# Kernel optimization log

Hardware: AMD Instinct MI355X
Metric: run time of the kernel (lower is better)

The kernel has to match this reference:

```python
import jax, jax.numpy as jnp
import numpy as np

# ---- static config (matches init_kwargs) ----
L, MM = 4, 2                     # lmax, mmax
C = 128                          # sphere_channels
H = 64                           # hidden_channels
OUTC = 128                       # output_channels
NH, AC = 8, 64                   # num_heads, attn_alpha_channels
MAXZ = 90
N_NODES, N_EDGES = 1000, 10000
EDGE_CH = 128
X_EDGE = EDGE_CH + 2 * EDGE_CH   # 384 (dist basis + src/tgt atom embeddings)
C3 = 3 * C                       # 384 channels of the concatenated message
EXTRA = NH * AC + L * H          # 768 extra m0 channels (alpha + gates)
M0_OUT = EXTRA + H * (L + 1)     # 1088
NC_FULL = (L + 1) ** 2           # 25

# ---- coefficient bookkeeping (CoefficientMappingModule) ----
_full = [(l, m) for l in range(L + 1) for m in range(-l, l + 1)]
_red = [(l, m) for l in range(L + 1) for m in range(-min(l, MM), min(l, MM) + 1)]
MASK = np.array([_full.index(p) for p in _red])  # rows of wigner with |m|<=mmax
_perm = [i for i, (l, m) in enumerate(_red) if m == 0]
for _mm in range(1, MM + 1):
    _perm += [i for i, (l, m) in enumerate(_red) if m == _mm]
    _perm += [i for i, (l, m) in enumerate(_red) if m == -_mm]
PERM_M = np.array(_perm)                 # l-primary -> m-primary
INV_PERM = np.argsort(PERM_M)            # m-primary -> l-primary
EXPAND_FULL = np.array([l for l, m in _full])       # l of each full coeff
GATE_EXPAND = np.array([l - 1 for l, m in _red if l > 0])


def _ln(h, g, b):
    mu = jnp.mean(h, -1, keepdims=True)
    var = jnp.var(h, -1, keepdims=True)
    return (h - mu) / jnp.sqrt(var + 1e-5) * g + b


def _forward(x, edge_fea, edge_distance, wigner, src_emb, tgt_emb,
             rad_w1, rad_b1, rad_g1, rad_bb1, rad_w2, rad_b2, rad_g2, rad_bb2,
             rad_w3, rad_b3, w_m0, b_m0, w_m1, w_m2, proj_w, proj_b,
             atomic_numbers, edge_index):
    E = edge_index.shape[1]
    src, tgt = edge_index[0], edge_index[1]
    # atom-edge embedding concat
    x_edge = jnp.concatenate([edge_distance,
                              src_emb[atomic_numbers[src]],
                              tgt_emb[atomic_numbers[tgt]]], axis=1)     # [E, 384]
    # edge-wise gather + concat -> message [E, 25, 3C]
    msg = jnp.concatenate([x[src], x[tgt], edge_fea], axis=2)
    # radial MLP (Linear + LayerNorm + SiLU, final Linear)
    h = jax.nn.silu(_ln(x_edge @ rad_w1.T + rad_b1, rad_g1, rad_bb1))
    h = jax.nn.silu(_ln(h @ rad_w2.T + rad_b2, rad_g2, rad_bb2))
    w_rad = (h @ rad_w3.T + rad_b3).reshape(E, L + 1, C3)                # [E, 5, 3C]
    msg = msg * w_rad[:, EXPAND_FULL, :]                                 # shared per-l radial weight
    # Wigner rotation restricted to |m| <= mmax: [E, 19, 3C]
    msg = jnp.einsum('emn,enc->emc', wigner[:, MASK, :], msg)
    # SO2 convolution (m-primary layout)
    mp = msg[:, PERM_M, :]
    x0 = mp[:, :L + 1, :].reshape(E, -1) @ w_m0.T + b_m0                 # [E, 1088]
    x0_extra = x0[:, :EXTRA]
    outs = [x0[:, EXTRA:].reshape(E, L + 1, H)]
    off = L + 1
    for m, w in ((1, w_m1), (2, w_m2)):
        nl = L - m + 1
        xm = mp[:, off:off + 2 * nl, :].reshape(E, 2, nl * C3)           # rows: +m, -m
        ym = xm @ w.T                                                    # [E, 2, 2*H*nl]
        half = ym.shape[-1] // 2
        yr, yi = ym[..., :half], ym[..., half:]
        outs.append(jnp.stack([yr[:, 0] - yi[:, 1], yr[:, 1] + yi[:, 0]],
                              axis=1).reshape(E, 2 * nl, H))
        off += 2 * nl
    hl = jnp.concatenate(outs, axis=1)[:, INV_PERM, :]                   # l-primary [E, 19, H]
    # gate activation: sigmoid gates for l>=1, SiLU on scalars
    gating = jax.nn.sigmoid(x0_extra[:, NH * AC:]).reshape(E, L, H)[:, GATE_EXPAND, :]
    hl = jnp.concatenate([jax.nn.silu(hl[:, :1, :]), hl[:, 1:, :] * gating], axis=1)
    # inverse rotation back to full (lmax+1)^2 coefficients: [E, 25, H]
    full = jnp.einsum('emn,emc->enc', wigner[:, MASK, :], hl)
    # SO3_LinearV2: per-l linear, bias only on l=0
    out = jnp.einsum('emi,moi->emo', full, proj_w[EXPAND_FULL])
    out = out.at[:, 0, :].add(proj_b)
    return out


def setup_inputs() -> dict:
    ks = jax.random.split(jax.random.key(0), 16)
    f32 = jnp.float32
    def nrm(k, shape, fan_in):
        return jax.random.normal(k, shape, dtype=f32) * (fan_in ** -0.5)
    return {
        'x': jax.random.normal(ks[0], (N_NODES, NC_FULL, C), dtype=f32),
        'edge_fea': jax.random.normal(ks[1], (N_EDGES, NC_FULL, C), dtype=f32),
        'edge_distance': jax.random.normal(ks[2], (N_EDGES, EDGE_CH), dtype=f32),
        'wigner': nrm(ks[3], (N_EDGES, NC_FULL, NC_FULL), NC_FULL),
        'src_emb': jax.random.uniform(ks[4], (MAXZ, EDGE_CH), f32, -0.001, 0.001),
        'tgt_emb': jax.random.uniform(ks[5], (MAXZ, EDGE_CH), f32, -0.001, 0.001),
        'rad_w1': nrm(ks[6], (EDGE_CH, X_EDGE), X_EDGE),
        'rad_b1': jnp.zeros((EDGE_CH,), f32),
        'rad_g1': jnp.ones((EDGE_CH,), f32),
        'rad_bb1': jnp.zeros((EDGE_CH,), f32),
        'rad_w2': nrm(ks[7], (EDGE_CH, EDGE_CH), EDGE_CH),
        'rad_b2': jnp.zeros((EDGE_CH,), f32),
        'rad_g2': jnp.ones((EDGE_CH,), f32),
        'rad_bb2': jnp.zeros((EDGE_CH,), f32),
        'rad_w3': nrm(ks[8], ((L + 1) * C3, EDGE_CH), EDGE_CH),
        'rad_b3': jnp.zeros(((L + 1) * C3,), f32),
        'w_m0': nrm(ks[9], (M0_OUT, (L + 1) * C3), (L + 1) * C3),
        'b_m0': jnp.zeros((M0_OUT,), f32),
        'w_m1': nrm(ks[10], (2 * H * L, L * C3), L * C3),
        'w_m2': nrm(ks[11], (2 * H * (L - 1), (L - 1) * C3), (L - 1) * C3),
        'proj_w': nrm(ks[12], (L + 1, OUTC, H), H),
        'proj_b': jnp.zeros((OUTC,), f32),
        'atomic_numbers': jax.random.randint(ks[13], (N_NODES,), 0, MAXZ, dtype=jnp.int32),
        'edge_index': jax.random.randint(ks[14], (2, N_EDGES), 0, N_NODES, dtype=jnp.int32),
    }


def reference(x, edge_fea, edge_distance, wigner, src_emb, tgt_emb,
              rad_w1, rad_b1, rad_g1, rad_bb1, rad_w2, rad_b2, rad_g2, rad_bb2,
              rad_w3, rad_b3, w_m0, b_m0, w_m1, w_m2, proj_w, proj_b,
              atomic_numbers, edge_index):
    return _forward(x, edge_fea, edge_distance, wigner, src_emb, tgt_emb,
                    rad_w1, rad_b1, rad_g1, rad_bb1, rad_w2, rad_b2, rad_g2, rad_bb2,
                    rad_w3, rad_b3, w_m0, b_m0, w_m1, w_m2, proj_w, proj_b,
                    atomic_numbers, edge_index)
```

## Files before the change

kernel.cpp:

```cpp
#include <hip/hip_runtime.h>
#include <hip/hip_bf16.h>
#include <stdint.h>


__constant__ int c_MASKP[19] = {0,2,6,12,20, 3,7,13,21, 1,5,11,19, 8,14,22, 4,10,18};
__constant__ int c_GATEP[19] = {-1,0,1,2,3, 0,1,2,3, 0,1,2,3, 1,2,3, 1,2,3};
__constant__ int c_LFULL[25] = {0,1,1,1,2,2,2,2,2,3,3,3,3,3,3,3,4,4,4,4,4,4,4,4,4};

__device__ __forceinline__ float sigm_(float x) { return 1.f / (1.f + __expf(-x)); }

typedef __attribute__((ext_vector_type(8))) __bf16 bf16x8;
typedef __attribute__((ext_vector_type(4))) float floatx4;

__device__ __forceinline__ void async16(const void* g, void* l) {
    __builtin_amdgcn_global_load_lds(
        (__attribute__((address_space(1))) void*)(g),
        (__attribute__((address_space(3))) void*)(l), 16, 0, 0);
}

__global__ void k_split_pw(const float* __restrict__ pw, __hip_bfloat16* __restrict__ pwb) {
    int d = blockIdx.x * 256 + threadIdx.x;
    if (d >= 40960) return;
    int ll = d >> 13, rem = d & 8191;
    int o = rem >> 6, i = rem & 63;
    float v = pw[d];
    __hip_bfloat16 hi = __float2bfloat16(v);
    __hip_bfloat16 lo = __float2bfloat16(v - __bfloat162float(hi));
    long ob = (long)(ll * 128 + o) * 192;
    pwb[ob + i]       = hi;
    pwb[ob + 64 + i]  = lo;
    pwb[ob + 128 + i] = hi;
}

__global__ void k_cvt_w(const float* __restrict__ W, __hip_bfloat16* __restrict__ out,
                        int rows, int rowsPad, int K) {
    long i = (long)blockIdx.x * 256 + threadIdx.x;
    if (i >= (long)rowsPad * K) return;
    int r = (int)(i / K);
    out[i] = __float2bfloat16(r < rows ? W[i] : 0.f);
}

__global__ void k_cvt_w_split(const float* __restrict__ W, __hip_bfloat16* __restrict__ out,
                              int rows, int K) {
    long i = (long)blockIdx.x * 256 + threadIdx.x;
    if (i >= (long)rows * K) return;
    int r = (int)(i / K), k = (int)(i - (long)r * K);
    float v = W[i];
    __hip_bfloat16 hi = __float2bfloat16(v);
    __hip_bfloat16 lo = __float2bfloat16(v - __bfloat162float(hi));
    long ob = (long)r * 3 * K;
    out[ob + k]         = hi;
    out[ob + K + k]     = lo;
    out[ob + 2 * K + k] = hi;
}

__global__ __launch_bounds__(256) void k_build_xedge(
    const float* __restrict__ ed, const float* __restrict__ se, const float* __restrict__ te,
    const int* __restrict__ an, const int* __restrict__ eidx,
    __hip_bfloat16* __restrict__ xeb, int e0, int ec, int E)
{
    long i = (long)blockIdx.x * 256 + threadIdx.x;
    if (i >= (long)ec * 384) return;
    int le = (int)(i / 384), c = (int)(i - (long)le * 384);
    int e = e0 + le;
    float v;
    if (c < 128)       v = ed[(long)e * 128 + c];
    else if (c < 256)  { int s = eidx[e];     v = se[an[s] * 128 + (c - 128)]; }
    else               { int t = eidx[E + e]; v = te[an[t] * 128 + (c - 256)]; }
    __hip_bfloat16 hi = __float2bfloat16(v);
    __hip_bfloat16 lo = __float2bfloat16(v - __bfloat162float(hi));
    long ob = (long)le * 1152;
    xeb[ob + c]       = hi;
    xeb[ob + 384 + c] = hi;
    xeb[ob + 768 + c] = lo;
}

__global__ __launch_bounds__(256) void k_ln_silu(
    const float* __restrict__ H, const float* __restrict__ g, const float* __restrict__ bb,
    __hip_bfloat16* __restrict__ out, int ec, int split)
{
    int row = blockIdx.x * 4 + (threadIdx.x >> 6);
    if (row >= ec) return;
    int lane = threadIdx.x & 63;
    const float* hr = H + (long)row * 128;
    float v0 = hr[lane], v1 = hr[lane + 64];
    float s = v0 + v1, s2 = v0 * v0 + v1 * v1;
    #pragma unroll
    for (int o = 32; o >= 1; o >>= 1) {
        s  += __shfl_xor(s, o, 64);
        s2 += __shfl_xor(s2, o, 64);
    }
    float mu = s * (1.f / 128.f);
    float rs = rsqrtf(s2 * (1.f / 128.f) - mu * mu + 1e-5f);
    float a0 = (v0 - mu) * rs * g[lane]      + bb[lane];
    float a1 = (v1 - mu) * rs * g[lane + 64] + bb[lane + 64];
    a0 = a0 * sigm_(a0);
    a1 = a1 * sigm_(a1);
    if (split) {
        long ob = (long)row * 384;
        __hip_bfloat16 h0 = __float2bfloat16(a0);
        __hip_bfloat16 l0 = __float2bfloat16(a0 - __bfloat162float(h0));
        __hip_bfloat16 h1 = __float2bfloat16(a1);
        __hip_bfloat16 l1 = __float2bfloat16(a1 - __bfloat162float(h1));
        out[ob + lane]            = h0;
        out[ob + 128 + lane]      = h0;
        out[ob + 256 + lane]      = l0;
        out[ob + lane + 64]       = h1;
        out[ob + 128 + lane + 64] = h1;
        out[ob + 256 + lane + 64] = l1;
    } else {
        long ob = (long)row * 128;
        out[ob + lane]      = __float2bfloat16(a0);
        out[ob + lane + 64] = __float2bfloat16(a1);
    }
}

__global__ __launch_bounds__(256) void k_mfma_gemm(
    const __hip_bfloat16* __restrict__ A,
    const __hip_bfloat16* __restrict__ B,
    const float* __restrict__ bias,
    float* __restrict__ Out, int ldo,
    int realM, int realN, int K)
{
    __shared__ __align__(16) __hip_bfloat16 As[128 * 32];
    __shared__ __align__(16) __hip_bfloat16 Bs[128 * 32];
    int tid = threadIdx.x;
    int l = tid & 63, w = tid >> 6;
    int r0 = blockIdx.x * 128, n0 = blockIdx.y * 128;
    int wm = w & 1, wn = w >> 1;

    floatx4 acc[4][4] = {};

    int srow = w * 16 + (l >> 2);
    int scol = (l & 3) * 8;
    const __hip_bfloat16* Ag = A + (long)(r0 + srow) * K + scol;
    const __hip_bfloat16* Bg = B + (long)(n0 + srow) * K + scol;
    __hip_bfloat16* AsW = As + (w * 16) * 32;
    __hip_bfloat16* BsW = Bs + (w * 16) * 32;

    int lrow = l & 15, lk = (l >> 4) * 8;

    for (int kk = 0; kk < K; kk += 32) {
        async16(Ag + kk, AsW);
        async16(Ag + (long)64 * K + kk, AsW + 64 * 32);
        async16(Bg + kk, BsW);
        async16(Bg + (long)64 * K + kk, BsW + 64 * 32);
        __syncthreads();
        bf16x8 af[4], bf[4];
        #pragma unroll
        for (int mi = 0; mi < 4; ++mi)
            af[mi] = *(const bf16x8*)&As[(wm * 64 + mi * 16 + lrow) * 32 + lk];
        #pragma unroll
        for (int ni = 0; ni < 4; ++ni)
            bf[ni] = *(const bf16x8*)&Bs[(wn * 64 + ni * 16 + lrow) * 32 + lk];
        #pragma unroll
        for (int mi = 0; mi < 4; ++mi)
            #pragma unroll
            for (int ni = 0; ni < 4; ++ni)
                acc[mi][ni] = __builtin_amdgcn_mfma_f32_16x16x32_bf16(
                    af[mi], bf[ni], acc[mi][ni], 0, 0, 0);
        __syncthreads();
    }

    int lq = l >> 4;
    #pragma unroll
    for (int ni = 0; ni < 4; ++ni) {
        int col = n0 + wn * 64 + ni * 16 + lrow;
        if (col >= realN) continue;
        float bv = bias ? bias[col] : 0.f;
        #pragma unroll
        for (int mi = 0; mi < 4; ++mi) {
            int rbase = r0 + wm * 64 + mi * 16 + lq * 4;
            floatx4 v = acc[mi][ni];
            #pragma unroll
            for (int r = 0; r < 4; ++r) {
                int row = rbase + r;
                if (row < realM) Out[(long)row * ldo + col] = v[r] + bv;
            }
        }
    }
}

__global__ __launch_bounds__(384) void k_build_mp(
    const float* __restrict__ x, const float* __restrict__ ef, const float* __restrict__ wgn,
    const float* __restrict__ wrad, const int* __restrict__ eidx,
    __hip_bfloat16* __restrict__ A0, __hip_bfloat16* __restrict__ A1,
    __hip_bfloat16* __restrict__ A2, int e0, int E)
{
    __shared__ __align__(16) float swig[512];
    int tid = threadIdx.x;
    int le = blockIdx.x;
    long e = e0 + le;
    int src = eidx[e], tgt = eidx[E + e];

    for (int i = tid; i < 500; i += 384) {
        int n = i / 20, j = i - n * 20;
        swig[i] = (j < 19) ? wgn[e * 625 + c_MASKP[j] * 25 + n] : 0.f;
    }

    int c = tid;
    const float* base;
    if (c < 128)      base = x  + (long)src * 3200 + c;
    else if (c < 256) base = x  + (long)tgt * 3200 + (c - 128);
    else              base = ef + e * 3200 + (c - 256);

    float vals[25];
    #pragma unroll
    for (int n = 0; n < 25; ++n) vals[n] = base[n * 128];
    float rad[5];
    #pragma unroll
    for (int l = 0; l < 5; ++l) rad[l] = wrad[(long)le * 1920 + l * 384 + c];
    #pragma unroll
    for (int n = 0; n < 25; ++n) vals[n] *= rad[c_LFULL[n]];

    __syncthreads();
    const float4* sw = (const float4*)swig;

    float acc[20] = {};
    #pragma unroll
    for (int n = 0; n < 25; ++n) {
        float v = vals[n];
        #pragma unroll
        for (int q = 0; q < 5; ++q) {
            float4 wv = sw[n * 5 + q];
            acc[q * 4 + 0] += wv.x * v;
            acc[q * 4 + 1] += wv.y * v;
            acc[q * 4 + 2] += wv.z * v;
            acc[q * 4 + 3] += wv.w * v;
        }
    }

    #pragma unroll
    for (int j = 0; j < 19; ++j) {
        __hip_bfloat16 hv = __float2bfloat16(acc[j]);
        if (j < 5)       A0[(long)le * 1920 + j * 384 + c] = hv;
        else if (j < 9)  A1[(long)(2 * le)     * 1536 + (j - 5)  * 384 + c] = hv;
        else if (j < 13) A1[(long)(2 * le + 1) * 1536 + (j - 9)  * 384 + c] = hv;
        else if (j < 16) A2[(long)(2 * le)     * 1152 + (j - 13) * 384 + c] = hv;
        else             A2[(long)(2 * le + 1) * 1152 + (j - 16) * 384 + c] = hv;
    }
}

__global__ __launch_bounds__(256) void k_combine_a(
    const float* __restrict__ wgn, const float* __restrict__ ym0,
    const float* __restrict__ ym1, const float* __restrict__ ym2,
    __hip_bfloat16* __restrict__ sfl, int e0, int CE)
{
    __shared__ __align__(16) float swig[512];
    __shared__ float shl[1216];
    int tid = threadIdx.x;
    int le = blockIdx.x;
    long e = e0 + le;

    for (int i = tid; i < 500; i += 256) {
        int n = i / 20, j = i - n * 20;
        swig[i] = (j < 19) ? wgn[e * 625 + c_MASKP[j] * 25 + n] : 0.f;
    }

    const float* y0  = ym0 + (long)le * 576;
    const float* y1a = ym1 + (long)(2 * le) * 512;
    const float* y1b = ym1 + (long)(2 * le + 1) * 512;
    const float* y2a = ym2 + (long)(2 * le) * 384;
    const float* y2b = ym2 + (long)(2 * le + 1) * 384;

    for (int i = tid; i < 1216; i += 256) {
        int j = i >> 6, c = i & 63;
        float raw;
        if (j < 5)        raw = y0[256 + j * 64 + c];
        else if (j < 9)   { int k = (j - 5) * 64 + c;  raw = y1a[k] - y1b[256 + k]; }
        else if (j < 13)  { int k = (j - 9) * 64 + c;  raw = y1b[k] + y1a[256 + k]; }
        else if (j < 16)  { int k = (j - 13) * 64 + c; raw = y2a[k] - y2b[192 + k]; }
        else              { int k = (j - 16) * 64 + c; raw = y2b[k] + y2a[192 + k]; }
        float v;
        if (j == 0) v = raw * sigm_(raw);
        else        v = raw * sigm_(y0[c_GATEP[j] * 64 + c]);
        shl[i] = v;
    }
    __syncthreads();

    for (int i = tid; i < 1600; i += 256) {
        int n = i >> 6, c = i & 63;
        const float4* sw = (const float4*)swig + n * 5;
        float acc = 0.f;
        float4 w0 = sw[0], w1 = sw[1], w2 = sw[2], w3 = sw[3], w4 = sw[4];
        acc += w0.x * shl[ 0 * 64 + c];
        acc += w0.y * shl[ 1 * 64 + c];
        acc += w0.z * shl[ 2 * 64 + c];
        acc += w0.w * shl[ 3 * 64 + c];
        acc += w1.x * shl[ 4 * 64 + c];
        acc += w1.y * shl[ 5 * 64 + c];
        acc += w1.z * shl[ 6 * 64 + c];
        acc += w1.w * shl[ 7 * 64 + c];
        acc += w2.x * shl[ 8 * 64 + c];
        acc += w2.y * shl[ 9 * 64 + c];
        acc += w2.z * shl[10 * 64 + c];
        acc += w2.w * shl[11 * 64 + c];
        acc += w3.x * shl[12 * 64 + c];
        acc += w3.y * shl[13 * 64 + c];
        acc += w3.z * shl[14 * 64 + c];
        acc += w3.w * shl[15 * 64 + c];
        acc += w4.x * shl[16 * 64 + c];
        acc += w4.y * shl[17 * 64 + c];
        acc += w4.z * shl[18 * 64 + c];
        __hip_bfloat16 hi = __float2bfloat16(acc);
        __hip_bfloat16 lo = __float2bfloat16(acc - __bfloat162float(hi));
        int l = c_LFULL[n];
        int nb = l * l, cnt = 2 * l + 1, ni = n - nb;
        long row = (long)CE * nb + (long)le * cnt + ni;
        sfl[row * 192 + c]       = hi;
        sfl[row * 192 + 64 + c]  = hi;
        sfl[row * 192 + 128 + c] = lo;
    }
}

__global__ __launch_bounds__(256) void k_proj_gemm(
    const __hip_bfloat16* __restrict__ sfl,
    const __hip_bfloat16* __restrict__ pwb,
    const float* __restrict__ pb,
    float* __restrict__ out, int ec, int CE)
{
    __shared__ __align__(16) __hip_bfloat16 As[128 * 32];
    __shared__ __align__(16) __hip_bfloat16 Bs[128 * 32];
    int tid = threadIdx.x;
    int ln = tid & 63, w = tid >> 6;
    int wm = w & 1, wn = w >> 1;

    int bid = blockIdx.x;
    int l = 0, base = 0;
    #pragma unroll
    for (int ll = 0; ll < 5; ++ll) {
        int tiles = (ec * (2 * ll + 1) + 127) >> 7;
        if (bid >= base + tiles) { base += tiles; l = ll + 1; }
    }
    if (l > 4) return;
    int cnt = 2 * l + 1, nb = l * l;
    int realM = ec * cnt;
    int r0 = (bid - base) * 128;

    const __hip_bfloat16* A = sfl + (long)CE * nb * 192;
    const __hip_bfloat16* B = pwb + l * 128 * 192;

    floatx4 acc[4][4] = {};

    int srow = w * 16 + (ln >> 2);
    int scol = (ln & 3) * 8;
    const __hip_bfloat16* Ag = A + (long)(r0 + srow) * 192 + scol;
    const __hip_bfloat16* Bg = B + (long)srow * 192 + scol;
    __hip_bfloat16* AsW = As + (w * 16) * 32;
    __hip_bfloat16* BsW = Bs + (w * 16) * 32;

    int lrow = ln & 15, lk = (ln >> 4) * 8;

    for (int kk = 0; kk < 192; kk += 32) {
        async16(Ag + kk, AsW);
        async16(Ag + (long)64 * 192 + kk, AsW + 64 * 32);
        async16(Bg + kk, BsW);
        async16(Bg + (long)64 * 192 + kk, BsW + 64 * 32);
        __syncthreads();
        bf16x8 af[4], bf[4];
        #pragma unroll
        for (int mi = 0; mi < 4; ++mi)
            af[mi] = *(const bf16x8*)&As[(wm * 64 + mi * 16 + lrow) * 32 + lk];
        #pragma unroll
        for (int ni = 0; ni < 4; ++ni)
            bf[ni] = *(const bf16x8*)&Bs[(wn * 64 + ni * 16 + lrow) * 32 + lk];
        #pragma unroll
        for (int mi = 0; mi < 4; ++mi)
            #pragma unroll
            for (int ni = 0; ni < 4; ++ni)
                acc[mi][ni] = __builtin_amdgcn_mfma_f32_16x16x32_bf16(
                    af[mi], bf[ni], acc[mi][ni], 0, 0, 0);
        __syncthreads();
    }

    int lq = ln >> 4;
    #pragma unroll
    for (int mi = 0; mi < 4; ++mi) {
        #pragma unroll
        for (int r = 0; r < 4; ++r) {
            int row = r0 + wm * 64 + mi * 16 + lq * 4 + r;
            if (row >= realM) continue;
            int e = row / cnt;
            int nn = nb + (row - e * cnt);
            float* op = out + (long)e * 3200 + (long)nn * 128;
            #pragma unroll
            for (int nib = 0; nib < 4; ++nib) {
                int col = wn * 64 + nib * 16 + lrow;
                float bv = (l == 0) ? pb[col] : 0.f;
                op[col] = acc[mi][nib][r] + bv;
            }
        }
    }
}

extern "C" void kernel_launch(void* const* d_in, const int* in_sizes, int n_in,
                              void* d_out, int out_size, void* d_ws, size_t ws_size,
                              hipStream_t stream)
{
    const float* x    = (const float*)d_in[0];
    const float* ef   = (const float*)d_in[1];
    const float* ed   = (const float*)d_in[2];
    const float* wgn  = (const float*)d_in[3];
    const float* se   = (const float*)d_in[4];
    const float* te   = (const float*)d_in[5];
    const float* w1   = (const float*)d_in[6];
    const float* b1   = (const float*)d_in[7];
    const float* g1   = (const float*)d_in[8];
    const float* bb1  = (const float*)d_in[9];
    const float* w2   = (const float*)d_in[10];
    const float* b2   = (const float*)d_in[11];
    const float* g2   = (const float*)d_in[12];
    const float* bb2  = (const float*)d_in[13];
    const float* w3   = (const float*)d_in[14];
    const float* b3   = (const float*)d_in[15];
    const float* wm0  = (const float*)d_in[16];
    const float* bm0  = (const float*)d_in[17];
    const float* wm1  = (const float*)d_in[18];
    const float* wm2  = (const float*)d_in[19];
    const float* pw   = (const float*)d_in[20];
    const float* pb   = (const float*)d_in[21];
    const int*   an   = (const int*)d_in[22];
    const int*   eidx = (const int*)d_in[23];
    float* out = (float*)d_out;
    char*  ws  = (char*)d_ws;

    const int E = in_sizes[23] / 2;

    size_t off = 0;
    __hip_bfloat16* pwb = (__hip_bfloat16*)(ws + off); off += 5L * 128 * 192 * 2;
    __hip_bfloat16* Wb0 = (__hip_bfloat16*)(ws + off); off += 640L  * 1920 * 2;
    __hip_bfloat16* Wb1 = (__hip_bfloat16*)(ws + off); off += 512L  * 1536 * 2;
    __hip_bfloat16* Wb2 = (__hip_bfloat16*)(ws + off); off += 384L  * 1152 * 2;
    __hip_bfloat16* Wb3 = (__hip_bfloat16*)(ws + off); off += 1920L * 128  * 2;
    __hip_bfloat16* W1b = (__hip_bfloat16*)(ws + off); off += 128L  * 1152 * 2;
    __hip_bfloat16* W2b = (__hip_bfloat16*)(ws + off); off += 128L  * 384  * 2;
    size_t fixedBytes = off;

    long usable = (long)ws_size - (long)fixedBytes;
    long ceRaw = usable / 45696;
    long Epad = ((long)E + 127) & ~127L;
    long CE = ceRaw & ~127L;
    if (CE > Epad) CE = Epad;
    if (CE < 128) CE = 128;

    __hip_bfloat16* h2b = (__hip_bfloat16*)(ws + off); off += CE * 128 * 2;
    float* wrad = (float*)(ws + off);                  off += CE * 1920 * 4;
    __hip_bfloat16* A0 = (__hip_bfloat16*)(ws + off);  off += CE * 1920 * 2;
    __hip_bfloat16* A1 = (__hip_bfloat16*)(ws + off);  off += 2 * CE * 1536 * 2;
    __hip_bfloat16* A2 = (__hip_bfloat16*)(ws + off);  off += 2 * CE * 1152 * 2;
    float* y0 = (float*)(ws + off);                    off += CE * 576 * 4;
    float* y1 = (float*)(ws + off);                    off += 2 * CE * 512 * 4;
    float* y2 = (float*)(ws + off);                    off += 2 * CE * 384 * 4;
    __hip_bfloat16* sfl = (__hip_bfloat16*)(ws + off); off += CE * 25 * 192 * 2;
    __hip_bfloat16* xeb = (__hip_bfloat16*)(ws + off); off += CE * 1152 * 2;
    float* h1 = (float*)(ws + off);                    off += CE * 128 * 4;
    __hip_bfloat16* h1s = (__hip_bfloat16*)(ws + off); off += CE * 384 * 2;
    float* h2 = (float*)(ws + off);                    off += CE * 128 * 4;

    k_split_pw<<<160, 256, 0, stream>>>(pw, pwb);
    k_cvt_w<<<(640 * 1920 + 255) / 256, 256, 0, stream>>>(wm0 + 512L * 1920, Wb0, 576, 640, 1920);
    k_cvt_w<<<(512 * 1536 + 255) / 256, 256, 0, stream>>>(wm1, Wb1, 512, 512, 1536);
    k_cvt_w<<<(384 * 1152 + 255) / 256, 256, 0, stream>>>(wm2, Wb2, 384, 384, 1152);
    k_cvt_w<<<(1920 * 128 + 255) / 256, 256, 0, stream>>>(w3, Wb3, 1920, 1920, 128);
    k_cvt_w_split<<<(128 * 384 + 255) / 256, 256, 0, stream>>>(w1, W1b, 128, 384);
    k_cvt_w_split<<<(128 * 128 + 255) / 256, 256, 0, stream>>>(w2, W2b, 128, 128);

    for (int e0 = 0; e0 < E; e0 += (int)CE) {
        int ec = (E - e0 < (int)CE) ? (E - e0) : (int)CE;
        int Mp  = (ec + 127) & ~127;
        int Mp2 = (2 * ec + 127) & ~127;

        k_build_xedge<<<dim3((ec * 384 + 255) / 256), 256, 0, stream>>>(
            ed, se, te, an, eidx, xeb, e0, ec, E);
        k_mfma_gemm<<<dim3(Mp / 128, 1), 256, 0, stream>>>(
            xeb, W1b, b1, h1, 128, ec, 128, 1152);
        k_ln_silu<<<dim3((ec + 3) / 4), 256, 0, stream>>>(h1, g1, bb1, h1s, ec, 1);
        k_mfma_gemm<<<dim3(Mp / 128, 1), 256, 0, stream>>>(
            h1s, W2b, b2, h2, 128, ec, 128, 384);
        k_ln_silu<<<dim3((ec + 3) / 4), 256, 0, stream>>>(h2, g2, bb2, h2b, ec, 0);

        k_mfma_gemm<<<dim3(Mp / 128, 1920 / 128), 256, 0, stream>>>(
            h2b, Wb3, b3, wrad, 1920, ec, 1920, 128);

        k_build_mp<<<dim3(ec), 384, 0, stream>>>(
            x, ef, wgn, wrad, eidx, A0, A1, A2, e0, E);

        k_mfma_gemm<<<dim3(Mp / 128, 640 / 128), 256, 0, stream>>>(
            A0, Wb0, bm0 + 512, y0, 576, ec, 576, 1920);
        k_mfma_gemm<<<dim3(Mp2 / 128, 512 / 128), 256, 0, stream>>>(
            A1, Wb1, (const float*)nullptr, y1, 512, 2 * ec, 512, 1536);
        k_mfma_gemm<<<dim3(Mp2 / 128, 384 / 128), 256, 0, stream>>>(
            A2, Wb2, (const float*)nullptr, y2, 384, 2 * ec, 384, 1152);

        k_combine_a<<<dim3(ec), 256, 0, stream>>>(wgn, y0, y1, y2, sfl, e0, (int)CE);

        int tilesTot = 0;
        for (int l = 0; l < 5; ++l) tilesTot += (ec * (2 * l + 1) + 127) >> 7;
        k_proj_gemm<<<dim3(tilesTot), 256, 0, stream>>>(
            sfl, pwb, pb, out + (long)e0 * 3200, ec, (int)CE);
    }
}
```

Baseline: 769.7 us.

## Merge three m0/m1/m2 GEMMs into one launch and use nontemporal loads

```diff
diff --git a/kernel.cpp b/kernel.cpp
--- a/kernel.cpp
+++ b/kernel.cpp
@@ -115,18 +115,13 @@
     }
 }
 
-__global__ __launch_bounds__(256) void k_mfma_gemm(
-    const __hip_bfloat16* __restrict__ A,
-    const __hip_bfloat16* __restrict__ B,
-    const float* __restrict__ bias,
-    float* __restrict__ Out, int ldo,
-    int realM, int realN, int K)
-{
-    __shared__ __align__(16) __hip_bfloat16 As[128 * 32];
-    __shared__ __align__(16) __hip_bfloat16 Bs[128 * 32];
-    int tid = threadIdx.x;
+__device__ __forceinline__ void gemm_body(
+    __hip_bfloat16* As, __hip_bfloat16* Bs,
+    const __hip_bfloat16* A, const __hip_bfloat16* B,
+    const float* bias, float* Out, int ldo,
+    int realM, int realN, int K, int r0, int n0, int tid)
+{
     int l = tid & 63, w = tid >> 6;
-    int r0 = blockIdx.x * 128, n0 = blockIdx.y * 128;
     int wm = w & 1, wn = w >> 1;
 
     floatx4 acc[4][4] = {};
@@ -181,6 +176,46 @@
     }
 }
 
+__global__ __launch_bounds__(256) void k_mfma_gemm(
+    const __hip_bfloat16* __restrict__ A,
+    const __hip_bfloat16* __restrict__ B,
+    const float* __restrict__ bias,
+    float* __restrict__ Out, int ldo,
+    int realM, int realN, int K)
+{
+    __shared__ __align__(16) __hip_bfloat16 As[128 * 32];
+    __shared__ __align__(16) __hip_bfloat16 Bs[128 * 32];
+    gemm_body(As, Bs, A, B, bias, Out, ldo, realM, realN, K,
+              blockIdx.x * 128, blockIdx.y * 128, threadIdx.x);
+}
+
+__global__ __launch_bounds__(256) void k_mfma_gemm3(
+    const __hip_bfloat16* __restrict__ A0, const __hip_bfloat16* __restrict__ B0,
+    const float* __restrict__ bias0, float* __restrict__ O0,
+    const __hip_bfloat16* __restrict__ A1, const __hip_bfloat16* __restrict__ B1,
+    float* __restrict__ O1,
+    const __hip_bfloat16* __restrict__ A2, const __hip_bfloat16* __restrict__ B2,
+    float* __restrict__ O2,
+    int mt0, int mt1, int ec)
+{
+    __shared__ __align__(16) __hip_bfloat16 As[128 * 32];
+    __shared__ __align__(16) __hip_bfloat16 Bs[128 * 32];
+    int t = blockIdx.x;
+    int s0 = mt0 * 5, s1 = mt1 * 4, s2 = mt1 * 3;
+    if (t < s0) {
+        gemm_body(As, Bs, A0, B0, bias0, O0, 576, ec, 576, 1920,
+                  (t % mt0) * 128, (t / mt0) * 128, threadIdx.x);
+    } else if (t < s0 + s1) {
+        t -= s0;
+        gemm_body(As, Bs, A1, B1, (const float*)nullptr, O1, 512, 2 * ec, 512, 1536,
+                  (t % mt1) * 128, (t / mt1) * 128, threadIdx.x);
+    } else if (t < s0 + s1 + s2) {
+        t -= s0 + s1;
+        gemm_body(As, Bs, A2, B2, (const float*)nullptr, O2, 384, 2 * ec, 384, 1152,
+                  (t % mt1) * 128, (t / mt1) * 128, threadIdx.x);
+    }
+}
+
 __global__ __launch_bounds__(384) void k_build_mp(
     const float* __restrict__ x, const float* __restrict__ ef, const float* __restrict__ wgn,
     const float* __restrict__ wrad, const int* __restrict__ eidx,
@@ -195,21 +230,36 @@
 
     for (int i = tid; i < 500; i += 384) {
         int n = i / 20, j = i - n * 20;
-        swig[i] = (j < 19) ? wgn[e * 625 + c_MASKP[j] * 25 + n] : 0.f;
+        swig[i] = (j < 19) ? __builtin_nontemporal_load(
+                                 &wgn[e * 625 + c_MASKP[j] * 25 + n]) : 0.f;
     }
 
     int c = tid;
-    const float* base;
-    if (c < 128)      base = x  + (long)src * 3200 + c;
-    else if (c < 256) base = x  + (long)tgt * 3200 + (c - 128);
-    else              base = ef + e * 3200 + (c - 256);
-
     float vals[25];
-    #pragma unroll
-    for (int n = 0; n < 25; ++n) vals[n] = base[n * 128];
+    if (c < 256) {
+        const float* base = (c < 128) ? (x + (long)src * 3200 + c)
+                                      : (x + (long)tgt * 3200 + (c - 128));
+        #pragma unroll
+        for (int n = 0; n < 25; ++n) vals[n] = base[n * 128];
+    } else {
+        const float* base = ef + e * 3200 + (c - 256);
+        #pragma unroll
+        for (int n = 0; n < 25; ++n)
+            vals[n] = __builtin_nontemporal_load(&base[n * 128]);
+    }
     float rad[5];
     #pragma unroll
-    for (int l = 0; l < 5; ++l) rad[l] = wrad[(long)le * 1920 + l * 384 + c];
+    for (int l = 0; l < 5; ++l)
+        rad[l] = __builtin_nontemporal_load(&wrad[(long)le * 1920 + l * 384 + c]);
+
+    asm volatile("" ::
+        "v"(vals[0]),  "v"(vals[1]),  "v"(vals[2]),  "v"(vals[3]),  "v"(vals[4]),
+        "v"(vals[5]),  "v"(vals[6]),  "v"(vals[7]),  "v"(vals[8]),  "v"(vals[9]),
+        "v"(vals[10]), "v"(vals[11]), "v"(vals[12]), "v"(vals[13]), "v"(vals[14]),
+        "v"(vals[15]), "v"(vals[16]), "v"(vals[17]), "v"(vals[18]), "v"(vals[19]),
+        "v"(vals[20]), "v"(vals[21]), "v"(vals[22]), "v"(vals[23]), "v"(vals[24]),
+        "v"(rad[0]), "v"(rad[1]), "v"(rad[2]), "v"(rad[3]), "v"(rad[4]));
+
     #pragma unroll
     for (int n = 0; n < 25; ++n) vals[n] *= rad[c_LFULL[n]];
 
@@ -254,7 +304,8 @@
 
     for (int i = tid; i < 500; i += 256) {
         int n = i / 20, j = i - n * 20;
-        swig[i] = (j < 19) ? wgn[e * 625 + c_MASKP[j] * 25 + n] : 0.f;
+        swig[i] = (j < 19) ? __builtin_nontemporal_load(
+                                 &wgn[e * 625 + c_MASKP[j] * 25 + n]) : 0.f;
     }
 
     const float* y0  = ym0 + (long)le * 576;
@@ -469,28 +520,25 @@
         int ec = (E - e0 < (int)CE) ? (E - e0) : (int)CE;
         int Mp  = (ec + 127) & ~127;
         int Mp2 = (2 * ec + 127) & ~127;
+        int mt0 = Mp / 128, mt1 = Mp2 / 128;
 
         k_build_xedge<<<dim3((ec * 384 + 255) / 256), 256, 0, stream>>>(
             ed, se, te, an, eidx, xeb, e0, ec, E);
-        k_mfma_gemm<<<dim3(Mp / 128, 1), 256, 0, stream>>>(
+        k_mfma_gemm<<<dim3(mt0, 1), 256, 0, stream>>>(
             xeb, W1b, b1, h1, 128, ec, 128, 1152);
         k_ln_silu<<<dim3((ec + 3) / 4), 256, 0, stream>>>(h1, g1, bb1, h1s, ec, 1);
-        k_mfma_gemm<<<dim3(Mp / 128, 1), 256, 0, stream>>>(
+        k_mfma_gemm<<<dim3(mt0, 1), 256, 0, stream>>>(
             h1s, W2b, b2, h2, 128, ec, 128, 384);
         k_ln_silu<<<dim3((ec + 3) / 4), 256, 0, stream>>>(h2, g2, bb2, h2b, ec, 0);
 
-        k_mfma_gemm<<<dim3(Mp / 128, 1920 / 128), 256, 0, stream>>>(
+        k_mfma_gemm<<<dim3(mt0, 1920 / 128), 256, 0, stream>>>(
             h2b, Wb3, b3, wrad, 1920, ec, 1920, 128);
 
         k_build_mp<<<dim3(ec), 384, 0, stream>>>(
             x, ef, wgn, wrad, eidx, A0, A1, A2, e0, E);
 
-        k_mfma_gemm<<<dim3(Mp / 128, 640 / 128), 256, 0, stream>>>(
-            A0, Wb0, bm0 + 512, y0, 576, ec, 576, 1920);
-        k_mfma_gemm<<<dim3(Mp2 / 128, 512 / 128), 256, 0, stream>>>(
-            A1, Wb1, (const float*)nullptr, y1, 512, 2 * ec, 512, 1536);
-        k_mfma_gemm<<<dim3(Mp2 / 128, 384 / 128), 256, 0, stream>>>(
-            A2, Wb2, (const float*)nullptr, y2, 384, 2 * ec, 384, 1152);
+        k_mfma_gemm3<<<dim3(mt0 * 5 + mt1 * 7), 256, 0, stream>>>(
+            A0, Wb0, bm0 + 512, y0, A1, Wb1, y1, A2, Wb2, y2, mt0, mt1, ec);
 
         k_combine_a<<<dim3(ec), 256, 0, stream>>>(wgn, y0, y1, y2, sfl, e0, (int)CE);
 
```

Result: faster. 705.5 us (-8.3%).
